# Kernel tuning notes

Hardware: AMD Instinct MI355X
Metric: run time of the kernel (lower is better)

The kernel has to match this reference:

```python
import jax, jax.numpy as jnp
import numpy as np

D_MODEL = 1024
N_HEAD = 16
D_K = D_MODEL // N_HEAD
D_FF = 2048
EPS = 1e-6
SCALE = np.sqrt(D_K).astype(np.float32)


def layer_norm(x, alpha, beta):
    # Faithful to source: unbiased std (ddof=1), eps added to std
    mean = jnp.mean(x, axis=-1, keepdims=True)
    std = jnp.std(x, axis=-1, keepdims=True, ddof=1) + EPS
    return alpha * (x - mean) / std + beta


def setup_inputs() -> dict:
    key = jax.random.key(0)
    ks = jax.random.split(key, 12)
    s = 0.02
    return {
        "x": jax.random.normal(ks[0], (4, 1024, D_MODEL), dtype=jnp.float32),
        "Wq": jax.random.normal(ks[1], (D_MODEL, D_MODEL), dtype=jnp.float32) * s,
        "bq": jax.random.normal(ks[2], (D_MODEL,), dtype=jnp.float32) * s,
        "Wo": jax.random.normal(ks[3], (D_MODEL, D_MODEL), dtype=jnp.float32) * s,
        "bo": jax.random.normal(ks[4], (D_MODEL,), dtype=jnp.float32) * s,
        "W1": jax.random.normal(ks[5], (D_MODEL, D_FF), dtype=jnp.float32) * s,
        "b1": jax.random.normal(ks[6], (D_FF,), dtype=jnp.float32) * s,
        "W2": jax.random.normal(ks[7], (D_FF, D_MODEL), dtype=jnp.float32) * s,
        "b2": jax.random.normal(ks[8], (D_MODEL,), dtype=jnp.float32) * s,
        "alpha": jnp.ones((D_MODEL,), dtype=jnp.float32),
        "beta": jnp.ones((D_MODEL,), dtype=jnp.float32),
    }


def reference(x, Wq, bq, Wo, bo, W1, b1, W2, b2, alpha, beta):
    b, s, d = x.shape
    # Source bug kept: q, k, v all use q_linear
    def proj(t):
        return (t @ Wq + bq).reshape(b, s, N_HEAD, D_K).transpose(0, 2, 1, 3)
    q = proj(x)  # [b,h,s,dk]
    k = proj(x)
    v = proj(x)
    scores = jnp.einsum('bhqd,bhkd->bhqk', q, k) / SCALE
    scores = jax.nn.softmax(scores, axis=-1)
    z = jnp.einsum('bhqk,bhkd->bhqd', scores, v)
    concat = z.transpose(0, 2, 1, 3).reshape(b, s, d)
    attn_out = concat @ Wo + bo
    x = layer_norm(x + attn_out, alpha, beta)
    ff = jax.nn.relu(x @ W1 + b1) @ W2 + b2
    x = layer_norm(x + ff, alpha, beta)  # source reuses norm_1
    return x
```

## Files before the change

kernel.cpp:

```cpp
#include <hip/hip_runtime.h>
#include <hip/hip_bf16.h>
#include <stdint.h>

#define TOK   4096
#define DMODEL 1024
#define DFF    2048
#define NHEAD  16
#define DK     64

typedef unsigned short u16;
typedef __attribute__((ext_vector_type(8))) short short8;
typedef __attribute__((ext_vector_type(4))) float f32x4;

typedef __attribute__((address_space(1))) void gvoid;
typedef __attribute__((address_space(3))) void lvoid;

#define QSCALE   0.35355339f
#define QUNSCALE 2.82842712f

__device__ __forceinline__ u16 f2b(float f) {
    uint32_t x = __builtin_bit_cast(uint32_t, f);
    x += 0x7FFFu + ((x >> 16) & 1u);
    return (u16)(x >> 16);
}
__device__ __forceinline__ float b2f(u16 u) {
    uint32_t x = ((uint32_t)u) << 16;
    return __builtin_bit_cast(float, x);
}
__device__ __forceinline__ uint32_t f2b2(float lo, float hi) {
    return (uint32_t)f2b(lo) | ((uint32_t)f2b(hi) << 16);
}

__device__ __forceinline__ void gload16(const void* g, void* l) {
    __builtin_amdgcn_global_load_lds((gvoid*)g, (lvoid*)l, 16, 0, 0);
}

__device__ __forceinline__ void cvt_tr_dev(
    const float* __restrict__ W, u16* __restrict__ Wt, int K, int N,
    int bx, int by, int tid, u16 (*T)[68])
{
    const int tx = tid & 15, ty = tid >> 4;
    const int n0 = bx * 64, k0 = by * 64;
#pragma unroll
    for (int i = 0; i < 4; i++) {
        int k = ty + i * 16;
        float4 v = *(const float4*)&W[(size_t)(k0 + k) * N + n0 + tx * 4];
        T[tx * 4 + 0][k] = f2b(v.x);
        T[tx * 4 + 1][k] = f2b(v.y);
        T[tx * 4 + 2][k] = f2b(v.z);
        T[tx * 4 + 3][k] = f2b(v.w);
    }
    __syncthreads();
#pragma unroll
    for (int i = 0; i < 4; i++) {
        int n = ty + i * 16;
        ushort4 o;
        o.x = T[n][tx * 4 + 0]; o.y = T[n][tx * 4 + 1];
        o.z = T[n][tx * 4 + 2]; o.w = T[n][tx * 4 + 3];
        *(ushort4*)&Wt[(size_t)(n0 + n) * K + k0 + tx * 4] = o;
    }
}

__global__ __launch_bounds__(256) void prep1(
    const float* __restrict__ Wq, u16* __restrict__ Wqt,
    const float* __restrict__ x, u16* __restrict__ xb)
{
    __shared__ u16 T[64][68];
    const int id = blockIdx.x, tid = threadIdx.x;
    if (id < 256) {
        cvt_tr_dev(Wq, Wqt, 1024, 1024, id & 15, id >> 4, tid, T);
    } else {
        size_t base = (size_t)(id - 256) * 1024 + tid;
#pragma unroll
        for (int j = 0; j < 4; j++) {
            float4 v = ((const float4*)x)[base + j * 256];
            ((uint2*)xb)[base + j * 256] =
                make_uint2(f2b2(v.x, v.y), f2b2(v.z, v.w));
        }
    }
}

template<int BM, int BN, bool RELU, bool OUTBF16, bool QOUT>
__global__ __launch_bounds__(256) void gemm_mfma(
    const u16* __restrict__ A, const u16* __restrict__ Bt,
    const float* __restrict__ bias, void* __restrict__ Cv,
    u16* __restrict__ CT, float oscale,
    int M, int N, int K)
{
    constexpr int MF = BM / 32;
    constexpr int NF = BN / 32;
    constexpr int ASTR = BM * 64;
    constexpr int BSTR = BN * 64;
    __shared__ __align__(16) u16 As[2 * ASTR];
    __shared__ __align__(16) u16 Bs[2 * BSTR];

    const int tid  = threadIdx.x;
    const int lane = tid & 63;
    const int wid  = tid >> 6;
    const int wm = wid >> 1, wn = wid & 1;
    const int frow = lane & 15, fk = lane >> 4;

    const int gx = N / BN;
    const int gy = M / BM;
    const int rpx = gy >> 3;
    const int L = blockIdx.x;
    const int xcd = L & 7, within = L >> 3;
    const int yy = xcd * rpx + within / gx;
    const int xx = within % gx;

    const int row0 = yy * BM;
    const int col0 = xx * BN;

    const u16* gA[MF]; u16* lA[MF];
    const u16* gB[NF]; u16* lB[NF];
#pragma unroll
    for (int inst = 0; inst < MF; inst++) {
        int s = inst * 256 + tid;
        int r = s >> 3;
        int kc = ((s & 7) ^ (r & 7)) * 8;
        gA[inst] = A + (size_t)(row0 + r) * K + kc;
        lA[inst] = As + inst * 2048 + wid * 512;
    }
#pragma unroll
    for (int inst = 0; inst < NF; inst++) {
        int s = inst * 256 + tid;
        int r = s >> 3;
        int kc = ((s & 7) ^ (r & 7)) * 8;
        gB[inst] = Bt + (size_t)(col0 + r) * K + kc;
        lB[inst] = Bs + inst * 2048 + wid * 512;
    }

    int aoff[MF][2], boff[NF][2];
#pragma unroll
    for (int m = 0; m < MF; m++) {
        int r = wm * (BM / 2) + m * 16 + frow;
#pragma unroll
        for (int kk = 0; kk < 2; kk++)
            aoff[m][kk] = r * 64 + (((kk << 2) + fk) ^ (r & 7)) * 8;
    }
#pragma unroll
    for (int n = 0; n < NF; n++) {
        int r = wn * (BN / 2) + n * 16 + frow;
#pragma unroll
        for (int kk = 0; kk < 2; kk++)
            boff[n][kk] = r * 64 + (((kk << 2) + fk) ^ (r & 7)) * 8;
    }

    f32x4 acc[MF][NF] = {};
    const int nT = K >> 6;

#pragma unroll
    for (int inst = 0; inst < MF; inst++) gload16(gA[inst], lA[inst]);
#pragma unroll
    for (int inst = 0; inst < NF; inst++) gload16(gB[inst], lB[inst]);
    __syncthreads();

    for (int t = 0; t < nT; t++) {
        const int cur = t & 1;
        if (t + 1 < nT) {
            const int k0 = (t + 1) << 6;
#pragma unroll
            for (int inst = 0; inst < MF; inst++)
                gload16(gA[inst] + k0, lA[inst] + (cur ^ 1) * ASTR);
#pragma unroll
            for (int inst = 0; inst < NF; inst++)
                gload16(gB[inst] + k0, lB[inst] + (cur ^ 1) * BSTR);
        }

        const u16* Ab = As + cur * ASTR;
        const u16* Bb = Bs + cur * BSTR;
        short8 a[MF][2], b[NF][2];
#pragma unroll
        for (int m = 0; m < MF; m++)
#pragma unroll
            for (int kk = 0; kk < 2; kk++)
                a[m][kk] = *(const short8*)(Ab + aoff[m][kk]);
#pragma unroll
        for (int n = 0; n < NF; n++)
#pragma unroll
            for (int kk = 0; kk < 2; kk++)
                b[n][kk] = *(const short8*)(Bb + boff[n][kk]);

#pragma unroll
        for (int m = 0; m < MF; m++)
#pragma unroll
            for (int n = 0; n < NF; n++)
#pragma unroll
                for (int kk = 0; kk < 2; kk++)
                    acc[m][n] = __builtin_amdgcn_mfma_f32_16x16x32_bf16(
                        a[m][kk], b[n][kk], acc[m][n], 0, 0, 0);

        __syncthreads();
    }

#pragma unroll
    for (int n = 0; n < NF; n++) {
        const int gcol = col0 + wn * (BN / 2) + n * 16 + frow;
        const float bv = bias[gcol];
#pragma unroll
        for (int m = 0; m < MF; m++) {
            const int grow0 = row0 + wm * (BM / 2) + m * 16 + fk * 4;
            float v[4];
#pragma unroll
            for (int i = 0; i < 4; i++) {
                v[i] = (acc[m][n][i] + bv) * oscale;
                if (RELU) v[i] = fmaxf(v[i], 0.0f);
                if (OUTBF16)
                    ((u16*)Cv)[(size_t)(grow0 + i) * N + gcol] = f2b(v[i]);
                else
                    ((float*)Cv)[(size_t)(grow0 + i) * N + gcol] = v[i];
            }
            if (QOUT) {
                const int hh = gcol >> 6, d = gcol & 63;
                const int bb = grow0 >> 10, sl = grow0 & 1023;
                *(uint2*)&CT[(((size_t)(bb * 16 + hh) * 64 + d) << 10) + sl] =
                    make_uint2(f2b2(v[0], v[1]), f2b2(v[2], v[3]));
            }
        }
    }
}

__global__ __launch_bounds__(256, 2) void attn_prepw(
    const u16* __restrict__ qb, const u16* __restrict__ qT,
    u16* __restrict__ zb,
    const float* __restrict__ Wo, const float* __restrict__ W1,
    const float* __restrict__ W2,
    u16* __restrict__ Wot, u16* __restrict__ W1t, u16* __restrict__ W2t)
{
    __shared__ __align__(16) u16 Ks[2][64 * 64];
    __shared__ __align__(16) u16 Kt[2][64 * 64];
    __shared__ __align__(16) u16 Ps[128 * 64];

    const int tid = threadIdx.x;
    const int id  = blockIdx.x;

    if (id >= 512) {
        u16 (*T)[68] = reinterpret_cast<u16 (*)[68]>(&Ks[0][0]);
        int t = id - 512;
        if (t < 256)       cvt_tr_dev(Wo, Wot, 1024, 1024, t & 15, t >> 4, tid, T);
        else if (t < 768)  { t -= 256; cvt_tr_dev(W1, W1t, 1024, 2048, t & 31, t >> 5, tid, T); }
        else               { t -= 768; cvt_tr_dev(W2, W2t, 2048, 1024, t & 15, t >> 4, tid, T); }
        return;
    }

    const int lane = tid & 63;
    const int w    = tid >> 6;
    const int frow = lane & 15, fk = lane >> 4;

    const int h  = id & 15;
    const int qt = (id >> 4) & 7;
    const int b  = id >> 7;
    const int q0 = qt * 128;

    const u16* qhead = qb + ((size_t)b * 1024) * 1024 + h * 64;
    const u16* thead = qT + ((size_t)(b * 16 + h) * 64) * 1024;

#pragma unroll
    for (int inst = 0; inst < 2; inst++) {
        int s = inst * 256 + tid, r = s >> 3, kc = ((s & 7) ^ (r & 7)) * 8;
        gload16(qhead + (size_t)r * 1024 + kc, Ks[0] + inst * 2048 + w * 512);
        gload16(thead + (size_t)r * 1024 + kc, Kt[0] + inst * 2048 + w * 512);
    }

    short8 qf[2][2];
#pragma unroll
    for (int m = 0; m < 2; m++) {
        int r = q0 + w * 32 + m * 16 + frow;
#pragma unroll
        for (int kk = 0; kk < 2; kk++)
            qf[m][kk] = *(const short8*)(qhead + (size_t)r * 1024 + kk * 32 + fk * 8);
    }

    float lp[2] = {};
    f32x4 o[2][4] = {};

    __syncthreads();

    for (int t = 0; t < 16; t++) {
        const int cur = t & 1;
        if (t < 15) {
            const int kv = (t + 1) * 64;
#pragma unroll
            for (int inst = 0; inst < 2; inst++) {
                int s = inst * 256 + tid, r = s >> 3, kc = ((s & 7) ^ (r & 7)) * 8;
                gload16(qhead + (size_t)(kv + r) * 1024 + kc,
                        Ks[cur ^ 1] + inst * 2048 + w * 512);
                gload16(thead + (size_t)r * 1024 + kv + kc,
                        Kt[cur ^ 1] + inst * 2048 + w * 512);
            }
        }

        short8 kf[4][2];
#pragma unroll
        for (int n = 0; n < 4; n++) {
            int r = n * 16 + frow;
#pragma unroll
            for (int kk = 0; kk < 2; kk++)
                kf[n][kk] = *(const short8*)(Ks[cur] + r * 64 +
                                             (((kk << 2) + fk) ^ (r & 7)) * 8);
        }
        f32x4 st[4][2] = {};
        __builtin_amdgcn_s_setprio(1);
#pragma unroll
        for (int nk = 0; nk < 4; nk++)
#pragma unroll
            for (int mq = 0; mq < 2; mq++)
#pragma unroll
                for (int kk = 0; kk < 2; kk++)
                    st[nk][mq] = __builtin_amdgcn_mfma_f32_16x16x32_bf16(
                        kf[nk][kk], qf[mq][kk], st[nk][mq], 0, 0, 0);
        __builtin_amdgcn_s_setprio(0);

#pragma unroll
        for (int mq = 0; mq < 2; mq++) {
            const int r = w * 32 + mq * 16 + frow;
            const int rb = r * 64, sw = (r & 7) << 3;
#pragma unroll
            for (int nk = 0; nk < 4; nk++) {
                float p0 = __expf(st[nk][mq][0]);
                float p1 = __expf(st[nk][mq][1]);
                float p2 = __expf(st[nk][mq][2]);
                float p3 = __expf(st[nk][mq][3]);
                lp[mq] += (p0 + p1) + (p2 + p3);
                *(uint2*)&Ps[rb + ((nk * 16 + fk * 4) ^ sw)] =
                    make_uint2(f2b2(p0, p1), f2b2(p2, p3));
            }
        }

        short8 pa[2][2], vf[4][2];
#pragma unroll
        for (int m = 0; m < 2; m++) {
            int r = w * 32 + m * 16 + frow;
#pragma unroll
            for (int kk = 0; kk < 2; kk++)
                pa[m][kk] = *(const short8*)(Ps + r * 64 +
                                             (((kk << 2) + fk) ^ (r & 7)) * 8);
        }
#pragma unroll
        for (int n = 0; n < 4; n++) {
            int r = n * 16 + frow;
#pragma unroll
            for (int kk = 0; kk < 2; kk++)
                vf[n][kk] = *(const short8*)(Kt[cur] + r * 64 +
                                             (((kk << 2) + fk) ^ (r & 7)) * 8);
        }
        __builtin_amdgcn_s_setprio(1);
#pragma unroll
        for (int m = 0; m < 2; m++)
#pragma unroll
            for (int n = 0; n < 4; n++)
#pragma unroll
                for (int kk = 0; kk < 2; kk++)
                    o[m][n] = __builtin_amdgcn_mfma_f32_16x16x32_bf16(
                        pa[m][kk], vf[n][kk], o[m][n], 0, 0, 0);
        __builtin_amdgcn_s_setprio(0);

        __syncthreads();
    }

#pragma unroll
    for (int mq = 0; mq < 2; mq++) {
        lp[mq] += __shfl_xor(lp[mq], 16);
        lp[mq] += __shfl_xor(lp[mq], 32);
    }
#pragma unroll
    for (int m = 0; m < 2; m++)
#pragma unroll
        for (int i = 0; i < 4; i++) {
            const float lfull = __shfl(lp[m], fk * 4 + i);
            const float rl = QUNSCALE / lfull;
            const size_t gr = (size_t)(b * 1024 + q0 + w * 32 + m * 16 + fk * 4 + i);
#pragma unroll
            for (int n = 0; n < 4; n++)
                zb[gr * 1024 + h * 64 + n * 16 + frow] = f2b(o[m][n][i] * rl);
        }
}

__device__ __forceinline__ float4 ld4(const float* p) { return *(const float4*)p; }
__device__ __forceinline__ float4 ld4(const u16* p) {
    ushort4 u = *(const ushort4*)p;
    return make_float4(b2f(u.x), b2f(u.y), b2f(u.z), b2f(u.w));
}
__device__ __forceinline__ void st4(float* p, float4 v) { *(float4*)p = v; }
__device__ __forceinline__ void st4(u16* p, float4 v) {
    *(uint2*)p = make_uint2(f2b2(v.x, v.y), f2b2(v.z, v.w));
}

template<typename TA, typename TB, typename TO>
__global__ __launch_bounds__(256) void add_ln(
    const TA* __restrict__ a, const TB* __restrict__ b,
    const float* __restrict__ alpha, const float* __restrict__ beta,
    TO* __restrict__ out)
{
    const int row = blockIdx.x;
    const int c = threadIdx.x * 4;
    float4 va = ld4(a + (size_t)row * DMODEL + c);
    float4 vb = ld4(b + (size_t)row * DMODEL + c);
    float v0 = va.x + vb.x, v1 = va.y + vb.y;
    float v2 = va.z + vb.z, v3 = va.w + vb.w;

    float sum = (v0 + v1) + (v2 + v3);
    float sq  = (v0 * v0 + v1 * v1) + (v2 * v2 + v3 * v3);
#pragma unroll
    for (int off = 32; off > 0; off >>= 1) {
        sum += __shfl_xor(sum, off);
        sq  += __shfl_xor(sq, off);
    }
    __shared__ float s1[4], s2[4];
    const int wid = threadIdx.x >> 6, lane = threadIdx.x & 63;
    if (lane == 0) { s1[wid] = sum; s2[wid] = sq; }
    __syncthreads();
    sum = (s1[0] + s1[1]) + (s1[2] + s1[3]);
    sq  = (s2[0] + s2[1]) + (s2[2] + s2[3]);

    const float mean = sum * (1.0f / 1024.0f);
    float var = (sq - 1024.0f * mean * mean) * (1.0f / 1023.0f);
    var = fmaxf(var, 0.0f);
    const float rdenom = 1.0f / (sqrtf(var) + 1e-6f);

    float4 al = *(const float4*)(alpha + c);
    float4 be = *(const float4*)(beta + c);
    float4 r;
    r.x = al.x * (v0 - mean) * rdenom + be.x;
    r.y = al.y * (v1 - mean) * rdenom + be.y;
    r.z = al.z * (v2 - mean) * rdenom + be.z;
    r.w = al.w * (v3 - mean) * rdenom + be.w;
    st4(out + (size_t)row * DMODEL + c, r);
}

extern "C" void kernel_launch(void* const* d_in, const int* in_sizes, int n_in,
                              void* d_out, int out_size, void* d_ws, size_t ws_size,
                              hipStream_t stream) {
    const float* x     = (const float*)d_in[0];
    const float* Wq    = (const float*)d_in[1];
    const float* bq    = (const float*)d_in[2];
    const float* Wo    = (const float*)d_in[3];
    const float* bo    = (const float*)d_in[4];
    const float* W1    = (const float*)d_in[5];
    const float* b1    = (const float*)d_in[6];
    const float* W2    = (const float*)d_in[7];
    const float* b2    = (const float*)d_in[8];
    const float* alpha = (const float*)d_in[9];
    const float* beta  = (const float*)d_in[10];

    char* base = (char*)d_ws;
    u16* Wqt = (u16*)base;
    u16* Wot = (u16*)(base + (2u  << 20));
    u16* W1t = (u16*)(base + (4u  << 20));
    u16* W2t = (u16*)(base + (8u  << 20));
    u16* zb  = (u16*)(base + (12u << 20));
    u16* x1b = zb;
    u16* qb  = (u16*)(base + (20u << 20));
    u16* g2  = qb;
    u16* qT  = (u16*)(base + (28u << 20));
    u16* g   = qT;
    u16* xb  = (u16*)(base + (36u << 20));
    u16* hb  = (u16*)(base + (36u << 20));

    dim3 blk(256);

    prep1<<<dim3(1280), blk, 0, stream>>>(Wq, Wqt, x, xb);

    gemm_mfma<128, 64, false, true, true><<<dim3(512), blk, 0, stream>>>(
        xb, Wqt, bq, qb, qT, QSCALE, TOK, 1024, 1024);
    attn_prepw<<<dim3(1792), blk, 0, stream>>>(
        qb, qT, zb, Wo, W1, W2, Wot, W1t, W2t);
    gemm_mfma<128, 64, false, true, false><<<dim3(512), blk, 0, stream>>>(
        zb, Wot, bo, g, nullptr, 1.0f, TOK, 1024, 1024);
    add_ln<u16, u16, u16><<<dim3(TOK), blk, 0, stream>>>(xb, g, alpha, beta, x1b);
    gemm_mfma<128, 128, true, true, false><<<dim3(512), blk, 0, stream>>>(
        x1b, W1t, b1, hb, nullptr, 1.0f, TOK, 2048, 1024);
    gemm_mfma<128, 64, false, true, false><<<dim3(512), blk, 0, stream>>>(
        hb, W2t, b2, g2, nullptr, 1.0f, TOK, 1024, 2048);
    add_ln<u16, u16, float><<<dim3(TOK), blk, 0, stream>>>(
        x1b, g2, alpha, beta, (float*)d_out);
}
```

Measured before the change: 143.8 us.

## Switch attention to 32x32x16 MFMA and keep P in registers

Rewrites the attention inner loop to use 32x32x16 bf16 MFMA tiles instead of 16x16x32. The S^T tile layout lets each lane hold a query column, so exponentiated probabilities are packed and exchanged across lane halves with shuffles rather than written to and re-read from a shared-memory P buffer. Dropping that LDS buffer cuts shared memory, and launch bounds are raised to target three blocks per CU. The risk is register pressure from the 16-wide accumulators under the tighter occupancy bound, plus the correctness of the shuffle-based operand remapping.

```diff
diff --git a/kernel.cpp b/kernel.cpp
--- a/kernel.cpp
+++ b/kernel.cpp
@@ -11,6 +11,8 @@
 typedef unsigned short u16;
 typedef __attribute__((ext_vector_type(8))) short short8;
 typedef __attribute__((ext_vector_type(4))) float f32x4;
+typedef __attribute__((ext_vector_type(16))) float f32x16;
+typedef __attribute__((ext_vector_type(4))) unsigned int u32x4;
 
 typedef __attribute__((address_space(1))) void gvoid;
 typedef __attribute__((address_space(3))) void lvoid;
@@ -220,7 +222,7 @@
     }
 }
 
-__global__ __launch_bounds__(256, 2) void attn_prepw(
+__global__ __launch_bounds__(256, 3) void attn_prepw(
     const u16* __restrict__ qb, const u16* __restrict__ qT,
     u16* __restrict__ zb,
     const float* __restrict__ Wo, const float* __restrict__ W1,
@@ -229,7 +231,6 @@
 {
     __shared__ __align__(16) u16 Ks[2][64 * 64];
     __shared__ __align__(16) u16 Kt[2][64 * 64];
-    __shared__ __align__(16) u16 Ps[128 * 64];
 
     const int tid = threadIdx.x;
     const int id  = blockIdx.x;
@@ -245,7 +246,8 @@
 
     const int lane = tid & 63;
     const int w    = tid >> 6;
-    const int frow = lane & 15, fk = lane >> 4;
+    const int l31  = lane & 31;
+    const int lh   = lane >> 5;
 
     const int h  = id & 15;
     const int qt = (id >> 4) & 7;
@@ -262,17 +264,14 @@
         gload16(thead + (size_t)r * 1024 + kc, Kt[0] + inst * 2048 + w * 512);
     }
 
-    short8 qf[2][2];
-#pragma unroll
-    for (int m = 0; m < 2; m++) {
-        int r = q0 + w * 32 + m * 16 + frow;
-#pragma unroll
-        for (int kk = 0; kk < 2; kk++)
-            qf[m][kk] = *(const short8*)(qhead + (size_t)r * 1024 + kk * 32 + fk * 8);
-    }
-
-    float lp[2] = {};
-    f32x4 o[2][4] = {};
+    short8 qf[4];
+#pragma unroll
+    for (int kk = 0; kk < 4; kk++)
+        qf[kk] = *(const short8*)(qhead +
+            (size_t)(q0 + w * 32 + l31) * 1024 + kk * 16 + lh * 8);
+
+    float lp = 0.0f;
+    f32x16 o[2] = {};
 
     __syncthreads();
 
@@ -290,89 +289,96 @@
             }
         }
 
-        short8 kf[4][2];
-#pragma unroll
-        for (int n = 0; n < 4; n++) {
-            int r = n * 16 + frow;
-#pragma unroll
-            for (int kk = 0; kk < 2; kk++)
-                kf[n][kk] = *(const short8*)(Ks[cur] + r * 64 +
-                                             (((kk << 2) + fk) ^ (r & 7)) * 8);
-        }
-        f32x4 st[4][2] = {};
+        short8 kf[2][4];
+#pragma unroll
+        for (int nk = 0; nk < 2; nk++) {
+            int r = nk * 32 + l31;
+#pragma unroll
+            for (int kk = 0; kk < 4; kk++)
+                kf[nk][kk] = *(const short8*)(Ks[cur] + r * 64 +
+                                              ((kk * 2 + lh) ^ (r & 7)) * 8);
+        }
+
+        f32x16 st[2] = {};
         __builtin_amdgcn_s_setprio(1);
 #pragma unroll
-        for (int nk = 0; nk < 4; nk++)
-#pragma unroll
-            for (int mq = 0; mq < 2; mq++)
-#pragma unroll
-                for (int kk = 0; kk < 2; kk++)
-                    st[nk][mq] = __builtin_amdgcn_mfma_f32_16x16x32_bf16(
-                        kf[nk][kk], qf[mq][kk], st[nk][mq], 0, 0, 0);
+        for (int nk = 0; nk < 2; nk++)
+#pragma unroll
+            for (int kk = 0; kk < 4; kk++)
+                st[nk] = __builtin_amdgcn_mfma_f32_32x32x16_bf16(
+                    kf[nk][kk], qf[kk], st[nk], 0, 0, 0);
         __builtin_amdgcn_s_setprio(0);
 
-#pragma unroll
-        for (int mq = 0; mq < 2; mq++) {
-            const int r = w * 32 + mq * 16 + frow;
-            const int rb = r * 64, sw = (r & 7) << 3;
-#pragma unroll
-            for (int nk = 0; nk < 4; nk++) {
-                float p0 = __expf(st[nk][mq][0]);
-                float p1 = __expf(st[nk][mq][1]);
-                float p2 = __expf(st[nk][mq][2]);
-                float p3 = __expf(st[nk][mq][3]);
-                lp[mq] += (p0 + p1) + (p2 + p3);
-                *(uint2*)&Ps[rb + ((nk * 16 + fk * 4) ^ sw)] =
-                    make_uint2(f2b2(p0, p1), f2b2(p2, p3));
+        uint32_t w0[2][4], w1[2][4];
+#pragma unroll
+        for (int nk = 0; nk < 2; nk++) {
+            float e[16];
+#pragma unroll
+            for (int r = 0; r < 16; r++) {
+                e[r] = __expf(st[nk][r]);
+                lp += e[r];
             }
-        }
-
-        short8 pa[2][2], vf[4][2];
-#pragma unroll
-        for (int m = 0; m < 2; m++) {
-            int r = w * 32 + m * 16 + frow;
-#pragma unroll
-            for (int kk = 0; kk < 2; kk++)
-                pa[m][kk] = *(const short8*)(Ps + r * 64 +
-                                             (((kk << 2) + fk) ^ (r & 7)) * 8);
-        }
-#pragma unroll
-        for (int n = 0; n < 4; n++) {
-            int r = n * 16 + frow;
-#pragma unroll
-            for (int kk = 0; kk < 2; kk++)
-                vf[n][kk] = *(const short8*)(Kt[cur] + r * 64 +
-                                             (((kk << 2) + fk) ^ (r & 7)) * 8);
-        }
+#pragma unroll
+            for (int g = 0; g < 4; g++) {
+                w0[nk][g] = f2b2(e[4 * g + 0], e[4 * g + 1]);
+                w1[nk][g] = f2b2(e[4 * g + 2], e[4 * g + 3]);
+            }
+        }
+
+        short8 pa[4];
+#pragma unroll
+        for (int kks = 0; kks < 4; kks++) {
+            const int nk = kks >> 1;
+            const int g  = (kks & 1) * 2;
+            uint32_t s0 = lh ? w0[nk][g] : w0[nk][g + 1];
+            uint32_t s1 = lh ? w1[nk][g] : w1[nk][g + 1];
+            uint32_t r0 = (uint32_t)__shfl_xor((int)s0, 32);
+            uint32_t r1 = (uint32_t)__shfl_xor((int)s1, 32);
+            u32x4 pw;
+            pw.x = lh ? r0 : w0[nk][g];
+            pw.y = lh ? r1 : w1[nk][g];
+            pw.z = lh ? w0[nk][g + 1] : r0;
+            pw.w = lh ? w1[nk][g + 1] : r1;
+            pa[kks] = __builtin_bit_cast(short8, pw);
+        }
+
+        short8 vf[2][4];
+#pragma unroll
+        for (int nf = 0; nf < 2; nf++) {
+            int r = nf * 32 + l31;
+#pragma unroll
+            for (int kks = 0; kks < 4; kks++)
+                vf[nf][kks] = *(const short8*)(Kt[cur] + r * 64 +
+                                               ((kks * 2 + lh) ^ (r & 7)) * 8);
+        }
+
         __builtin_amdgcn_s_setprio(1);
 #pragma unroll
-        for (int m = 0; m < 2; m++)
-#pragma unroll
-            for (int n = 0; n < 4; n++)
-#pragma unroll
-                for (int kk = 0; kk < 2; kk++)
-                    o[m][n] = __builtin_amdgcn_mfma_f32_16x16x32_bf16(
-                        pa[m][kk], vf[n][kk], o[m][n], 0, 0, 0);
+        for (int nf = 0; nf < 2; nf++)
+#pragma unroll
+            for (int kks = 0; kks < 4; kks++)
+                o[nf] = __builtin_amdgcn_mfma_f32_32x32x16_bf16(
+                    pa[kks], vf[nf][kks], o[nf], 0, 0, 0);
         __builtin_amdgcn_s_setprio(0);
 
         __syncthreads();
     }
 
-#pragma unroll
-    for (int mq = 0; mq < 2; mq++) {
-        lp[mq] += __shfl_xor(lp[mq], 16);
-        lp[mq] += __shfl_xor(lp[mq], 32);
-    }
-#pragma unroll
-    for (int m = 0; m < 2; m++)
-#pragma unroll
-        for (int i = 0; i < 4; i++) {
-            const float lfull = __shfl(lp[m], fk * 4 + i);
-            const float rl = QUNSCALE / lfull;
-            const size_t gr = (size_t)(b * 1024 + q0 + w * 32 + m * 16 + fk * 4 + i);
-#pragma unroll
-            for (int n = 0; n < 4; n++)
-                zb[gr * 1024 + h * 64 + n * 16 + frow] = f2b(o[m][n][i] * rl);
+    lp += __shfl_xor(lp, 32);
+    const float rl = QUNSCALE / lp;
+    float rlq[16];
+#pragma unroll
+    for (int r = 0; r < 16; r++) {
+        const int qrow = (r & 3) + 8 * (r >> 2) + 4 * lh;
+        rlq[r] = __shfl(rl, qrow);
+    }
+#pragma unroll
+    for (int nf = 0; nf < 2; nf++)
+#pragma unroll
+        for (int r = 0; r < 16; r++) {
+            const int qrow = (r & 3) + 8 * (r >> 2) + 4 * lh;
+            const size_t gr = (size_t)(b * 1024 + q0 + w * 32 + qrow);
+            zb[gr * 1024 + h * 64 + nf * 32 + l31] = f2b(o[nf][r] * rlq[r]);
         }
 }
 
```

New measurement: 146.1 us. About the same (+1.5%).
